# Optimization experiments

Hardware: AMD Instinct MI355X
Metric: run time of the kernel (lower is better)

Reference implementation:

```python
import jax, jax.numpy as jnp
import numpy as np

WS = (5, 5, 5, 5)  # 4D window

def _rel_index(ws):
    # faithful port of WindowAttention.relative_bias_4d
    coords = np.stack(np.meshgrid(*[np.arange(w) for w in ws], indexing='ij'))  # (4, H,W,Hs,Ws)
    flat = coords.reshape(len(ws), -1)                       # (4, N)
    rel = (flat[:, :, None] - flat[:, None, :]).transpose(1, 2, 0).astype(np.int64)  # (N, N, 4)
    rel = rel + np.array([ws[0] - 1, ws[1] - 1, ws[2] - 1, ws[3] - 1])
    rel[..., 0] *= (2 * ws[0] - 1) ** 3
    rel[..., 1] *= (2 * ws[1] - 1) ** 2
    rel[..., 2] *= (2 * ws[2] - 1)
    return rel.sum(-1)  # (N, N), values in [0, (2w-1)^4)


def setup_inputs() -> dict:
    key = jax.random.key(0)
    ks = jax.random.split(key, 7)
    dim, heads = 128, 4
    B_, nW = 64, 32
    N = 5 ** 4  # 625
    tbl = (2 * 5 - 1) ** 4  # 6561
    inp = {
        'x': jax.random.normal(ks[0], (B_, N, dim), jnp.float32),
        'mask': jax.random.normal(ks[1], (nW, N, N), jnp.float32),
        'qkv_w': jax.random.normal(ks[2], (3 * dim, dim), jnp.float32) * 0.02,
        'qkv_b': jax.random.normal(ks[3], (3 * dim,), jnp.float32) * 0.02,
        'proj_w': jax.random.normal(ks[4], (dim, dim), jnp.float32) * 0.02,
        'proj_b': jax.random.normal(ks[5], (dim,), jnp.float32) * 0.02,
        'bias_table': jax.random.normal(ks[6], (tbl, heads), jnp.float32) * 0.02,
        'rel_index': jnp.asarray(_rel_index(WS), jnp.int32),
    }
    return inp


def reference(x, mask, qkv_w, qkv_b, proj_w, proj_b, bias_table, rel_index):
    B_, N, C = x.shape
    H = bias_table.shape[-1]
    D = C // H
    scale = D ** -0.5
    # qkv projection -> (3, B_, H, N, D)
    qkv = (x @ qkv_w.T + qkv_b).reshape(B_, N, 3, H, D).transpose(2, 0, 3, 1, 4)
    q, k, v = qkv[0], qkv[1], qkv[2]
    attn = jnp.einsum('bhnd,bhmd->bhnm', q * scale, k)       # (B_, H, N, N)
    bias = bias_table[rel_index].transpose(2, 0, 1)          # (H, N, N)
    attn = attn + bias[None]
    nW = mask.shape[0]
    attn = attn.reshape(B_ // nW, nW, H, N, N) + mask[None, :, None]
    attn = jax.nn.softmax(attn.reshape(B_, H, N, N), axis=-1)
    out = jnp.einsum('bhnm,bhmd->bhnd', attn, v)             # (B_, H, N, D)
    out = out.transpose(0, 2, 1, 3).reshape(B_, N, C)
    return out @ proj_w.T + proj_b
```

## Files before the change

### kernel.cpp

```cpp
#include <hip/hip_runtime.h>
#include <stdint.h>

typedef __attribute__((ext_vector_type(8))) __bf16 bf16x8;
typedef __attribute__((ext_vector_type(4))) __bf16 bf16x4;
typedef __attribute__((ext_vector_type(4))) float f32x4;

#define DEV __device__ __forceinline__
#define LOG2E 1.4426950408889634f
#define SCALE 0.17677669529663687f

static constexpr size_t OFF_Q     = 0;
static constexpr size_t OFF_K     = 10485760;
static constexpr size_t OFF_VT    = 20971520;
static constexpr size_t OFF_O     = 31457280;
static constexpr size_t OFF_BIASP = 41697280;
static constexpr size_t OFF_WBF   = 44974080;

DEV bf16x8 cvt8(const float* p) {
  f32x4 a = *(const f32x4*)p;
  f32x4 b = *(const f32x4*)(p + 4);
  bf16x8 r;
  r[0]=(__bf16)a[0]; r[1]=(__bf16)a[1]; r[2]=(__bf16)a[2]; r[3]=(__bf16)a[3];
  r[4]=(__bf16)b[0]; r[5]=(__bf16)b[1]; r[6]=(__bf16)b[2]; r[7]=(__bf16)b[3];
  return r;
}

DEV f32x4 mfma16(bf16x8 a, bf16x8 b, f32x4 c) {
  return __builtin_amdgcn_mfma_f32_16x16x32_bf16(a, b, c, 0, 0, 0);
}

DEV void gload16(const float* g, float* l) {
  typedef const __attribute__((address_space(1))) uint32_t* gp_t;
  typedef __attribute__((address_space(3))) uint32_t* lp_t;
  __builtin_amdgcn_global_load_lds((gp_t)g, (lp_t)l, 16, 0, 0);
}

__global__ __launch_bounds__(256) void k_prep(const float* __restrict__ table,
                                              const int* __restrict__ rel,
                                              __bf16* __restrict__ bp,
                                              __bf16* __restrict__ qp,
                                              __bf16* __restrict__ kp,
                                              __bf16* __restrict__ vp,
                                              const float* __restrict__ wq,
                                              const float* __restrict__ wp,
                                              __bf16* __restrict__ wbf) {
  int blk = blockIdx.x;
  if (blk < 1600) {
    int t = blk * 256 + threadIdx.x;
    int h = t / 102400, rem = t % 102400;
    int i = rem / 160, j4 = (rem % 160) * 4;
    bf16x4 v;
    if (i < 625) {
      #pragma unroll
      for (int r = 0; r < 4; ++r) {
        int j = j4 + r;
        v[r] = (j < 625) ? (__bf16)(table[(size_t)rel[(size_t)i * 625 + j] * 4 + h] * LOG2E)
                         : (__bf16)0.f;
      }
    } else {
      v[0] = v[1] = v[2] = v[3] = (__bf16)0.f;
    }
    *(bf16x4*)(bp + ((size_t)h * 640 + i) * 640 + j4) = v;
  } else if (blk < 2560) {
    int t = (blk - 1600) * 256 + threadIdx.x;
    const int PAD1 = 256 * 15 * 32;
    if (t < PAD1) {
      int bh = t / 480, rem = t % 480;
      int row = 625 + rem / 32, d = rem & 31;
      size_t idx = ((size_t)bh * 640 + row) * 32 + d;
      qp[idx] = (__bf16)0.f;
      kp[idx] = (__bf16)0.f;
    } else {
      t -= PAD1;
      if (t < PAD1) {
        int bh = t / 480, rem = t % 480;
        int d = rem / 15, col = 625 + rem % 15;
        vp[((size_t)bh * 32 + d) * 640 + col] = (__bf16)0.f;
      }
    }
  } else {
    int t = (blk - 2560) * 256 + threadIdx.x;
    if (t < 49152) wbf[t] = (__bf16)wq[t];
    else           wbf[t] = (__bf16)wp[t - 49152];
  }
}

__global__ __launch_bounds__(256) void k_qkv(const float* __restrict__ x,
                                             const __bf16* __restrict__ wbf,
                                             const float* __restrict__ bias,
                                             __bf16* __restrict__ qp,
                                             __bf16* __restrict__ kp,
                                             __bf16* __restrict__ vp) {
  int lane = threadIdx.x & 63, wv = threadIdx.x >> 6;
  int g = lane >> 4, l15 = lane & 15;
  int row0 = (blockIdx.x * 4 + wv) * 16;

  bf16x8 a[4];
  #pragma unroll
  for (int ks = 0; ks < 4; ++ks)
    a[ks] = cvt8(x + (size_t)(row0 + l15) * 128 + ks * 32 + g * 8);

  #pragma unroll 1
  for (int nf = 0; nf < 24; ++nf) {
    f32x4 acc = {0.f, 0.f, 0.f, 0.f};
    int col = nf * 16 + l15;
    #pragma unroll
    for (int ks = 0; ks < 4; ++ks) {
      bf16x8 bfr = *(const bf16x8*)(wbf + (size_t)col * 128 + ks * 32 + g * 8);
      acc = mfma16(a[ks], bfr, acc);
    }
    float bv = bias[col];
    int which = nf >> 3;
    int h = (col >> 5) & 3, d = col & 31;
    #pragma unroll
    for (int r = 0; r < 4; ++r) {
      int row = row0 + 4 * g + r;
      int b_ = row / 625;
      int n = row - b_ * 625;
      float v = acc[r] + bv;
      size_t bh = (size_t)b_ * 4 + h;
      if (which == 0)       qp[(bh * 640 + n) * 32 + d] = (__bf16)(v * (SCALE * LOG2E));
      else if (which == 1)  kp[(bh * 640 + n) * 32 + d] = (__bf16)v;
      else                  vp[(bh * 32 + d) * 640 + n] = (__bf16)v;
    }
  }
}

__global__ __launch_bounds__(256, 4) void k_attn6(const __bf16* __restrict__ qball,
                                                  const __bf16* __restrict__ kball,
                                                  const __bf16* __restrict__ vball,
                                                  __bf16* __restrict__ oball,
                                                  const __bf16* __restrict__ biasp,
                                                  const float* __restrict__ maskraw) {
  __shared__ __align__(16) float Mbuf[2][32 * 32];
  __shared__ __align__(16) unsigned short Pl[4][32 * 56];

  const int tid = threadIdx.x;
  const int lane = tid & 63, wv = tid >> 6;
  const int g = lane >> 4, l15 = lane & 15;

  const int bid = blockIdx.x;
  const int xcd = bid & 7, s = bid >> 3;
  const int w = xcd + 8 * (s & 3);
  const int r_ = s >> 2;
  const int o = r_ & 1, chunk = r_ >> 1;
  const int b = o * 32 + w;
  const int h = wv;
  const size_t bh = (size_t)b * 4 + h;
  const int i0 = chunk * 32;

  const __bf16* qp = qball + bh * (640 * 32);
  const __bf16* kp = kball + bh * (640 * 32);
  const __bf16* vp = vball + bh * (32 * 640);
  const float* maskw = maskraw + (size_t)w * 390625;

  const __bf16* kbase  = kp + (size_t)l15 * 32 + g * 8;
  const __bf16* vbase0 = vp + (size_t)l15 * 640 + 8 * g;
  const __bf16* vbase1 = vp + (size_t)(16 + l15) * 640 + 8 * g;
  const __bf16* brow0  = biasp + (size_t)h * 409600 + (size_t)(i0 + l15) * 640 + 4 * g;
  const __bf16* brow1  = brow0 + 16 * 640;

  const int il_s = wv * 8 + (lane >> 3);
  const int gr_s = (lane & 7) ^ (il_s & 7);
  int row_s = i0 + il_s; row_s = row_s < 625 ? row_s : 624;
  const float* msrc = maskw + (size_t)row_s * 625 + gr_s * 4;
  float* mdst0 = &Mbuf[0][wv * 256];
  float* mdst1 = &Mbuf[1][wv * 256];

  bf16x8 aq0 = *(const bf16x8*)(qp + (size_t)(i0 + l15) * 32 + g * 8);
  bf16x8 aq1 = *(const bf16x8*)(qp + (size_t)(i0 + 16 + l15) * 32 + g * 8);

  unsigned short* Prow0 = &Pl[wv][l15 * 56];
  unsigned short* Prow1 = &Pl[wv][(16 + l15) * 56];

  f32x4 O00 = {0,0,0,0}, O01 = {0,0,0,0}, O10 = {0,0,0,0}, O11 = {0,0,0,0};
  float L0 = 0.f, L1 = 0.f;

  bf16x8 K0, K1;
  bf16x4 B00, B01, B10, B11;

  gload16(msrc, mdst0);
  K0  = *(const bf16x8*)(kbase);
  K1  = *(const bf16x8*)(kbase + 512);
  B00 = *(const bf16x4*)(brow0);
  B01 = *(const bf16x4*)(brow0 + 16);
  B10 = *(const bf16x4*)(brow1);
  B11 = *(const bf16x4*)(brow1 + 16);
  __syncthreads();

#define CORE(BUF, T)                                                           \
  {                                                                            \
                                       \
    bf16x8 v0 = *(const bf16x8*)(vbase0 + (T) * 32);                           \
    bf16x8 v1 = *(const bf16x8*)(vbase1 + (T) * 32);                           \
    const int swz = (l15 & 7) << 2;                                            \
    f32x4 c00 = *(const f32x4*)&Mbuf[BUF][l15 * 32 + ((4 * g) ^ swz)];         \
    f32x4 c01 = *(const f32x4*)&Mbuf[BUF][l15 * 32 + ((16 + 4 * g) ^ swz)];    \
    f32x4 c10 = *(const f32x4*)&Mbuf[BUF][(16 + l15) * 32 + ((4 * g) ^ swz)];  \
    f32x4 c11 = *(const f32x4*)&Mbuf[BUF][(16 + l15) * 32 + ((16 + 4 * g) ^ swz)]; \
    _Pragma("unroll")                                                          \
    for (int r = 0; r < 4; ++r) {                                              \
      c00[r] = fmaf(c00[r], LOG2E, (float)B00[r]);                             \
      c01[r] = fmaf(c01[r], LOG2E, (float)B01[r]);                             \
      c10[r] = fmaf(c10[r], LOG2E, (float)B10[r]);                             \
      c11[r] = fmaf(c11[r], LOG2E, (float)B11[r]);                             \
    }                                                                          \
    f32x4 S00 = mfma16(K0, aq0, c00);                                          \
    f32x4 S01 = mfma16(K1, aq0, c01);                                          \
    f32x4 S10 = mfma16(K0, aq1, c10);                                          \
    f32x4 S11 = mfma16(K1, aq1, c11);                                          \
    if ((T) < 19) {   \
      K0  = *(const bf16x8*)(kbase + (size_t)((T) + 1) * 1024);                \
      K1  = *(const bf16x8*)(kbase + (size_t)((T) + 1) * 1024 + 512);          \
      B00 = *(const bf16x4*)(brow0 + ((T) + 1) * 32);                          \
      B01 = *(const bf16x4*)(brow0 + ((T) + 1) * 32 + 16);                     \
      B10 = *(const bf16x4*)(brow1 + ((T) + 1) * 32);                          \
      B11 = *(const bf16x4*)(brow1 + ((T) + 1) * 32 + 16);                     \
    }                                                                          \
    float ps0 = 0.f, ps1 = 0.f;                                                \
    bf16x4 pk00, pk01, pk10, pk11;                                             \
    _Pragma("unroll")                                                          \
    for (int r = 0; r < 4; ++r) {                                              \
      float p00 = exp2f(S00[r]);                                               \
      float p01 = exp2f(S01[r]);                                               \
      float p10 = exp2f(S10[r]);                                               \
      float p11 = exp2f(S11[r]);                                               \
      ps0 += p00 + p01;                                                        \
      ps1 += p10 + p11;                                                        \
      pk00[r] = (__bf16)p00;                                                   \
      pk01[r] = (__bf16)p01;                                                   \
      pk10[r] = (__bf16)p10;                                                   \
      pk11[r] = (__bf16)p11;                                                   \
    }                                                                          \
    L0 += ps0; L1 += ps1;                                                      \
    *(bf16x4*)(Prow0 + 4 * g) = pk00;                                          \
    *(bf16x4*)(Prow0 + 16 + 4 * g) = pk01;                                     \
    *(bf16x4*)(Prow1 + 4 * g) = pk10;                                          \
    *(bf16x4*)(Prow1 + 16 + 4 * g) = pk11;                                     \
    bf16x8 pa0 = *(const bf16x8*)(Prow0 + 8 * g);                              \
    bf16x8 pa1 = *(const bf16x8*)(Prow1 + 8 * g);                              \
    O00 = mfma16(pa0, v0, O00);                                                \
    O01 = mfma16(pa0, v1, O01);                                                \
    O10 = mfma16(pa1, v0, O10);                                                \
    O11 = mfma16(pa1, v1, O11);                                                \
  }

  #pragma unroll 1
  for (int t = 0; t < 18; ++t) {
    gload16(msrc + (size_t)(t + 1) * 32, (t & 1) ? mdst0 : mdst1);
    CORE(t & 1, t)
    __syncthreads();
  }
  CORE(0, 18)

  {
    bf16x8 v0 = *(const bf16x8*)(vbase0 + 19 * 32);
    bf16x8 v1 = *(const bf16x8*)(vbase1 + 19 * 32);
    int i_a = i0 + l15;       int ir0 = i_a < 625 ? i_a : 624;
    int i_b = i0 + 16 + l15;  int ir1 = i_b < 625 ? i_b : 624;
    const float* mr0 = maskw + (size_t)ir0 * 625;
    const float* mr1 = maskw + (size_t)ir1 * 625;
    f32x4 c, S00, S01, S10, S11;
    #pragma unroll
    for (int r = 0; r < 4; ++r)
      c[r] = fmaf(mr0[608 + 4 * g + r], LOG2E, (float)B00[r]);
    S00 = mfma16(K0, aq0, c);
    #pragma unroll
    for (int r = 0; r < 4; ++r) {
      int j = 624 + 4 * g + r;
      c[r] = (j < 625) ? fmaf(mr0[j], LOG2E, (float)B01[r]) : -1.0e30f;
    }
    S01 = mfma16(K1, aq0, c);
    #pragma unroll
    for (int r = 0; r < 4; ++r)
      c[r] = fmaf(mr1[608 + 4 * g + r], LOG2E, (float)B10[r]);
    S10 = mfma16(K0, aq1, c);
    #pragma unroll
    for (int r = 0; r < 4; ++r) {
      int j = 624 + 4 * g + r;
      c[r] = (j < 625) ? fmaf(mr1[j], LOG2E, (float)B11[r]) : -1.0e30f;
    }
    S11 = mfma16(K1, aq1, c);

    float ps0 = 0.f, ps1 = 0.f;
    bf16x4 pk00, pk01, pk10, pk11;
    #pragma unroll
    for (int r = 0; r < 4; ++r) {
      float p00 = exp2f(S00[r]);
      float p01 = exp2f(S01[r]);
      float p10 = exp2f(S10[r]);
      float p11 = exp2f(S11[r]);
      ps0 += p00 + p01;
      ps1 += p10 + p11;
      pk00[r] = (__bf16)p00;
      pk01[r] = (__bf16)p01;
      pk10[r] = (__bf16)p10;
      pk11[r] = (__bf16)p11;
    }
    L0 += ps0; L1 += ps1;
    *(bf16x4*)(Prow0 + 4 * g) = pk00;
    *(bf16x4*)(Prow0 + 16 + 4 * g) = pk01;
    *(bf16x4*)(Prow1 + 4 * g) = pk10;
    *(bf16x4*)(Prow1 + 16 + 4 * g) = pk11;
    bf16x8 pa0 = *(const bf16x8*)(Prow0 + 8 * g);
    bf16x8 pa1 = *(const bf16x8*)(Prow1 + 8 * g);
    O00 = mfma16(pa0, v0, O00);
    O01 = mfma16(pa0, v1, O01);
    O10 = mfma16(pa1, v0, O10);
    O11 = mfma16(pa1, v1, O11);
  }
#undef CORE

  L0 += __shfl_xor(L0, 16); L0 += __shfl_xor(L0, 32);
  L1 += __shfl_xor(L1, 16); L1 += __shfl_xor(L1, 32);
  float inv0 = 1.0f / L0, inv1 = 1.0f / L1;
  f32x4 iv0, iv1;
  #pragma unroll
  for (int r = 0; r < 4; ++r) {
    iv0[r] = __shfl(inv0, 4 * g + r);
    iv1[r] = __shfl(inv1, 4 * g + r);
  }
  #pragma unroll
  for (int r = 0; r < 4; ++r) {
    int ia = i0 + 4 * g + r;
    if (ia < 625) {
      size_t base = ((size_t)b * 625 + ia) * 128 + h * 32;
      oball[base + l15]      = (__bf16)(O00[r] * iv0[r]);
      oball[base + 16 + l15] = (__bf16)(O01[r] * iv0[r]);
    }
    int ib = i0 + 16 + 4 * g + r;
    if (ib < 625) {
      size_t base = ((size_t)b * 625 + ib) * 128 + h * 32;
      oball[base + l15]      = (__bf16)(O10[r] * iv1[r]);
      oball[base + 16 + l15] = (__bf16)(O11[r] * iv1[r]);
    }
  }
}

__global__ __launch_bounds__(256) void k_proj(const __bf16* __restrict__ obf,
                                              const __bf16* __restrict__ wbf,
                                              const float* __restrict__ bias,
                                              float* __restrict__ out) {
  int lane = threadIdx.x & 63, wv = threadIdx.x >> 6;
  int g = lane >> 4, l15 = lane & 15;
  int row0 = (blockIdx.x * 4 + wv) * 16;

  bf16x8 a[4];
  #pragma unroll
  for (int ks = 0; ks < 4; ++ks)
    a[ks] = *(const bf16x8*)(obf + (size_t)(row0 + l15) * 128 + ks * 32 + g * 8);

  #pragma unroll 1
  for (int nf = 0; nf < 8; ++nf) {
    f32x4 acc = {0.f, 0.f, 0.f, 0.f};
    int col = nf * 16 + l15;
    #pragma unroll
    for (int ks = 0; ks < 4; ++ks) {
      bf16x8 bfr = *(const bf16x8*)(wbf + (size_t)col * 128 + ks * 32 + g * 8);
      acc = mfma16(a[ks], bfr, acc);
    }
    float bv = bias[col];
    #pragma unroll
    for (int r = 0; r < 4; ++r)
      out[(size_t)(row0 + 4 * g + r) * 128 + col] = acc[r] + bv;
  }
}

extern "C" void kernel_launch(void* const* d_in, const int* in_sizes, int n_in,
                              void* d_out, int out_size, void* d_ws, size_t ws_size,
                              hipStream_t stream) {
  (void)in_sizes; (void)n_in; (void)out_size; (void)ws_size;
  const float* x      = (const float*)d_in[0];
  const float* mask   = (const float*)d_in[1];
  const float* qkv_w  = (const float*)d_in[2];
  const float* qkv_b  = (const float*)d_in[3];
  const float* proj_w = (const float*)d_in[4];
  const float* proj_b = (const float*)d_in[5];
  const float* table  = (const float*)d_in[6];
  const int*   rel    = (const int*)d_in[7];
  char* ws = (char*)d_ws;
  float* out = (float*)d_out;

  __bf16* qp    = (__bf16*)(ws + OFF_Q);
  __bf16* kp    = (__bf16*)(ws + OFF_K);
  __bf16* vp    = (__bf16*)(ws + OFF_VT);
  __bf16* obf   = (__bf16*)(ws + OFF_O);
  __bf16* biasp = (__bf16*)(ws + OFF_BIASP);
  __bf16* wbf   = (__bf16*)(ws + OFF_WBF);

  k_prep<<<2816, 256, 0, stream>>>(table, rel, biasp, qp, kp, vp, qkv_w, proj_w, wbf);
  k_qkv<<<625, 256, 0, stream>>>(x, wbf, qkv_b, qp, kp, vp);
  k_attn6<<<1280, 256, 0, stream>>>(qp, kp, vp, obf, biasp, mask);
  k_proj<<<625, 256, 0, stream>>>(obf, wbf + 49152, proj_b, out);
}
```

Baseline: 162.1 us.

## Load mask directly into registers and permute bias layout for 8-wide loads

The attention kernel stops staging the mask tile through double-buffered LDS with async global-to-LDS loads and per-tile block barriers. Each lane now reads its mask values straight from global memory into registers, prefetching one tile ahead. The precomputed bias array is reordered so each lane fetches a single 8-element bf16 vector per row instead of two 4-element loads. This removes the block-wide synchronisation and LDS traffic, at the cost of more register pressure and less coalesced mask reads.

New measurement: 157.2 us. -3.1%, faster.

```diff
diff --git a/kernel.cpp b/kernel.cpp
--- a/kernel.cpp
+++ b/kernel.cpp
@@ -27,12 +27,6 @@
 
 DEV f32x4 mfma16(bf16x8 a, bf16x8 b, f32x4 c) {
   return __builtin_amdgcn_mfma_f32_16x16x32_bf16(a, b, c, 0, 0, 0);
-}
-
-DEV void gload16(const float* g, float* l) {
-  typedef const __attribute__((address_space(1))) uint32_t* gp_t;
-  typedef __attribute__((address_space(3))) uint32_t* lp_t;
-  __builtin_amdgcn_global_load_lds((gp_t)g, (lp_t)l, 16, 0, 0);
 }
 
 __global__ __launch_bounds__(256) void k_prep(const float* __restrict__ table,
@@ -48,19 +42,22 @@
   if (blk < 1600) {
     int t = blk * 256 + threadIdx.x;
     int h = t / 102400, rem = t % 102400;
-    int i = rem / 160, j4 = (rem % 160) * 4;
+    int i = rem / 160, q = rem % 160;
+    int e0 = q * 4;
+    int tile = e0 >> 5;
+    int ein = e0 & 31;
+    int g = ein >> 3, s0 = ein & 7;
     bf16x4 v;
-    if (i < 625) {
-      #pragma unroll
-      for (int r = 0; r < 4; ++r) {
-        int j = j4 + r;
-        v[r] = (j < 625) ? (__bf16)(table[(size_t)rel[(size_t)i * 625 + j] * 4 + h] * LOG2E)
-                         : (__bf16)0.f;
-      }
-    } else {
-      v[0] = v[1] = v[2] = v[3] = (__bf16)0.f;
-    }
-    *(bf16x4*)(bp + ((size_t)h * 640 + i) * 640 + j4) = v;
+    #pragma unroll
+    for (int s2 = 0; s2 < 4; ++s2) {
+      int s = s0 + s2;
+      int col = 4 * g + (s < 4 ? s : s + 12);
+      int j = tile * 32 + col;
+      v[s2] = (i < 625 && j < 625)
+                ? (__bf16)(table[(size_t)rel[(size_t)i * 625 + j] * 4 + h] * LOG2E)
+                : (__bf16)0.f;
+    }
+    *(bf16x4*)(bp + ((size_t)h * 640 + i) * 640 + e0) = v;
   } else if (blk < 2560) {
     int t = (blk - 1600) * 256 + threadIdx.x;
     const int PAD1 = 256 * 15 * 32;
@@ -126,13 +123,12 @@
   }
 }
 
-__global__ __launch_bounds__(256, 4) void k_attn6(const __bf16* __restrict__ qball,
+__global__ __launch_bounds__(256, 4) void k_attn8(const __bf16* __restrict__ qball,
                                                   const __bf16* __restrict__ kball,
                                                   const __bf16* __restrict__ vball,
                                                   __bf16* __restrict__ oball,
                                                   const __bf16* __restrict__ biasp,
                                                   const float* __restrict__ maskraw) {
-  __shared__ __align__(16) float Mbuf[2][32 * 32];
   __shared__ __align__(16) unsigned short Pl[4][32 * 56];
 
   const int tid = threadIdx.x;
@@ -157,15 +153,13 @@
   const __bf16* kbase  = kp + (size_t)l15 * 32 + g * 8;
   const __bf16* vbase0 = vp + (size_t)l15 * 640 + 8 * g;
   const __bf16* vbase1 = vp + (size_t)(16 + l15) * 640 + 8 * g;
-  const __bf16* brow0  = biasp + (size_t)h * 409600 + (size_t)(i0 + l15) * 640 + 4 * g;
+  const __bf16* brow0  = biasp + (size_t)h * 409600 + (size_t)(i0 + l15) * 640 + g * 8;
   const __bf16* brow1  = brow0 + 16 * 640;
 
-  const int il_s = wv * 8 + (lane >> 3);
-  const int gr_s = (lane & 7) ^ (il_s & 7);
-  int row_s = i0 + il_s; row_s = row_s < 625 ? row_s : 624;
-  const float* msrc = maskw + (size_t)row_s * 625 + gr_s * 4;
-  float* mdst0 = &Mbuf[0][wv * 256];
-  float* mdst1 = &Mbuf[1][wv * 256];
+  int ia = i0 + l15;       const int ir0 = ia < 625 ? ia : 624;
+  int ib_ = i0 + 16 + l15; const int ir1 = ib_ < 625 ? ib_ : 624;
+  const float* mrow0 = maskw + (size_t)ir0 * 625 + 4 * g;
+  const float* mrow1 = maskw + (size_t)ir1 * 625 + 4 * g;
 
   bf16x8 aq0 = *(const bf16x8*)(qp + (size_t)(i0 + l15) * 32 + g * 8);
   bf16x8 aq1 = *(const bf16x8*)(qp + (size_t)(i0 + 16 + l15) * 32 + g * 8);
@@ -177,110 +171,44 @@
   float L0 = 0.f, L1 = 0.f;
 
   bf16x8 K0, K1;
-  bf16x4 B00, B01, B10, B11;
-
-  gload16(msrc, mdst0);
+  bf16x8 B0, B1;
+  f32x4 C00, C01, C10, C11;
+
+  C00 = *(const f32x4*)(mrow0);
+  C01 = *(const f32x4*)(mrow0 + 16);
+  C10 = *(const f32x4*)(mrow1);
+  C11 = *(const f32x4*)(mrow1 + 16);
   K0  = *(const bf16x8*)(kbase);
   K1  = *(const bf16x8*)(kbase + 512);
-  B00 = *(const bf16x4*)(brow0);
-  B01 = *(const bf16x4*)(brow0 + 16);
-  B10 = *(const bf16x4*)(brow1);
-  B11 = *(const bf16x4*)(brow1 + 16);
-  __syncthreads();
-
-#define CORE(BUF, T)                                                           \
-  {                                                                            \
-                                       \
-    bf16x8 v0 = *(const bf16x8*)(vbase0 + (T) * 32);                           \
-    bf16x8 v1 = *(const bf16x8*)(vbase1 + (T) * 32);                           \
-    const int swz = (l15 & 7) << 2;                                            \
-    f32x4 c00 = *(const f32x4*)&Mbuf[BUF][l15 * 32 + ((4 * g) ^ swz)];         \
-    f32x4 c01 = *(const f32x4*)&Mbuf[BUF][l15 * 32 + ((16 + 4 * g) ^ swz)];    \
-    f32x4 c10 = *(const f32x4*)&Mbuf[BUF][(16 + l15) * 32 + ((4 * g) ^ swz)];  \
-    f32x4 c11 = *(const f32x4*)&Mbuf[BUF][(16 + l15) * 32 + ((16 + 4 * g) ^ swz)]; \
-    _Pragma("unroll")                                                          \
-    for (int r = 0; r < 4; ++r) {                                              \
-      c00[r] = fmaf(c00[r], LOG2E, (float)B00[r]);                             \
-      c01[r] = fmaf(c01[r], LOG2E, (float)B01[r]);                             \
-      c10[r] = fmaf(c10[r], LOG2E, (float)B10[r]);                             \
-      c11[r] = fmaf(c11[r], LOG2E, (float)B11[r]);                             \
-    }                                                                          \
-    f32x4 S00 = mfma16(K0, aq0, c00);                                          \
-    f32x4 S01 = mfma16(K1, aq0, c01);                                          \
-    f32x4 S10 = mfma16(K0, aq1, c10);                                          \
-    f32x4 S11 = mfma16(K1, aq1, c11);                                          \
-    if ((T) < 19) {   \
-      K0  = *(const bf16x8*)(kbase + (size_t)((T) + 1) * 1024);                \
-      K1  = *(const bf16x8*)(kbase + (size_t)((T) + 1) * 1024 + 512);          \
-      B00 = *(const bf16x4*)(brow0 + ((T) + 1) * 32);                          \
-      B01 = *(const bf16x4*)(brow0 + ((T) + 1) * 32 + 16);                     \
-      B10 = *(const bf16x4*)(brow1 + ((T) + 1) * 32);                          \
-      B11 = *(const bf16x4*)(brow1 + ((T) + 1) * 32 + 16);                     \
-    }                                                                          \
-    float ps0 = 0.f, ps1 = 0.f;                                                \
-    bf16x4 pk00, pk01, pk10, pk11;                                             \
-    _Pragma("unroll")                                                          \
-    for (int r = 0; r < 4; ++r) {                                              \
-      float p00 = exp2f(S00[r]);                                               \
-      float p01 = exp2f(S01[r]);                                               \
-      float p10 = exp2f(S10[r]);                                               \
-      float p11 = exp2f(S11[r]);                                               \
-      ps0 += p00 + p01;                                                        \
-      ps1 += p10 + p11;                                                        \
-      pk00[r] = (__bf16)p00;                                                   \
-      pk01[r] = (__bf16)p01;                                                   \
-      pk10[r] = (__bf16)p10;                                                   \
-      pk11[r] = (__bf16)p11;                                                   \
-    }                                                                          \
-    L0 += ps0; L1 += ps1;                                                      \
-    *(bf16x4*)(Prow0 + 4 * g) = pk00;                                          \
-    *(bf16x4*)(Prow0 + 16 + 4 * g) = pk01;                                     \
-    *(bf16x4*)(Prow1 + 4 * g) = pk10;                                          \
-    *(bf16x4*)(Prow1 + 16 + 4 * g) = pk11;                                     \
-    bf16x8 pa0 = *(const bf16x8*)(Prow0 + 8 * g);                              \
-    bf16x8 pa1 = *(const bf16x8*)(Prow1 + 8 * g);                              \
-    O00 = mfma16(pa0, v0, O00);                                                \
-    O01 = mfma16(pa0, v1, O01);                                                \
-    O10 = mfma16(pa1, v0, O10);                                                \
-    O11 = mfma16(pa1, v1, O11);                                                \
-  }
+  B0  = *(const bf16x8*)(brow0);
+  B1  = *(const bf16x8*)(brow1);
 
   #pragma unroll 1
-  for (int t = 0; t < 18; ++t) {
-    gload16(msrc + (size_t)(t + 1) * 32, (t & 1) ? mdst0 : mdst1);
-    CORE(t & 1, t)
-    __syncthreads();
-  }
-  CORE(0, 18)
-
-  {
-    bf16x8 v0 = *(const bf16x8*)(vbase0 + 19 * 32);
-    bf16x8 v1 = *(const bf16x8*)(vbase1 + 19 * 32);
-    int i_a = i0 + l15;       int ir0 = i_a < 625 ? i_a : 624;
-    int i_b = i0 + 16 + l15;  int ir1 = i_b < 625 ? i_b : 624;
-    const float* mr0 = maskw + (size_t)ir0 * 625;
-    const float* mr1 = maskw + (size_t)ir1 * 625;
-    f32x4 c, S00, S01, S10, S11;
-    #pragma unroll
-    for (int r = 0; r < 4; ++r)
-      c[r] = fmaf(mr0[608 + 4 * g + r], LOG2E, (float)B00[r]);
-    S00 = mfma16(K0, aq0, c);
-    #pragma unroll
-    for (int r = 0; r < 4; ++r) {
-      int j = 624 + 4 * g + r;
-      c[r] = (j < 625) ? fmaf(mr0[j], LOG2E, (float)B01[r]) : -1.0e30f;
-    }
-    S01 = mfma16(K1, aq0, c);
-    #pragma unroll
-    for (int r = 0; r < 4; ++r)
-      c[r] = fmaf(mr1[608 + 4 * g + r], LOG2E, (float)B10[r]);
-    S10 = mfma16(K0, aq1, c);
-    #pragma unroll
-    for (int r = 0; r < 4; ++r) {
-      int j = 624 + 4 * g + r;
-      c[r] = (j < 625) ? fmaf(mr1[j], LOG2E, (float)B11[r]) : -1.0e30f;
-    }
-    S11 = mfma16(K1, aq1, c);
+  for (int t = 0; t < 19; ++t) {
+    bf16x8 v0 = *(const bf16x8*)(vbase0 + t * 32);
+    bf16x8 v1 = *(const bf16x8*)(vbase1 + t * 32);
+    f32x4 c00, c01, c10, c11;
+    #pragma unroll
+    for (int r = 0; r < 4; ++r) {
+      c00[r] = fmaf(C00[r], LOG2E, (float)B0[r]);
+      c01[r] = fmaf(C01[r], LOG2E, (float)B0[4 + r]);
+      c10[r] = fmaf(C10[r], LOG2E, (float)B1[r]);
+      c11[r] = fmaf(C11[r], LOG2E, (float)B1[4 + r]);
+    }
+    f32x4 S00 = mfma16(K0, aq0, c00);
+    f32x4 S01 = mfma16(K1, aq0, c01);
+    f32x4 S10 = mfma16(K0, aq1, c10);
+    f32x4 S11 = mfma16(K1, aq1, c11);
+    if (t < 18) {
+      C00 = *(const f32x4*)(mrow0 + (t + 1) * 32);
+      C01 = *(const f32x4*)(mrow0 + (t + 1) * 32 + 16);
+      C10 = *(const f32x4*)(mrow1 + (t + 1) * 32);
+      C11 = *(const f32x4*)(mrow1 + (t + 1) * 32 + 16);
+    }
+    K0 = *(const bf16x8*)(kbase + (size_t)(t + 1) * 1024);
+    K1 = *(const bf16x8*)(kbase + (size_t)(t + 1) * 1024 + 512);
+    B0 = *(const bf16x8*)(brow0 + (t + 1) * 32);
+    B1 = *(const bf16x8*)(brow1 + (t + 1) * 32);
 
     float ps0 = 0.f, ps1 = 0.f;
     bf16x4 pk00, pk01, pk10, pk11;
@@ -309,7 +237,61 @@
     O10 = mfma16(pa1, v0, O10);
     O11 = mfma16(pa1, v1, O11);
   }
-#undef CORE
+
+  {
+    bf16x8 v0 = *(const bf16x8*)(vbase0 + 19 * 32);
+    bf16x8 v1 = *(const bf16x8*)(vbase1 + 19 * 32);
+    const float* mr0 = maskw + (size_t)ir0 * 625;
+    const float* mr1 = maskw + (size_t)ir1 * 625;
+    f32x4 c, S00, S01, S10, S11;
+    #pragma unroll
+    for (int r = 0; r < 4; ++r)
+      c[r] = fmaf(mr0[608 + 4 * g + r], LOG2E, (float)B0[r]);
+    S00 = mfma16(K0, aq0, c);
+    #pragma unroll
+    for (int r = 0; r < 4; ++r) {
+      int j = 624 + 4 * g + r;
+      c[r] = (j < 625) ? fmaf(mr0[j], LOG2E, (float)B0[4 + r]) : -1.0e30f;
+    }
+    S01 = mfma16(K1, aq0, c);
+    #pragma unroll
+    for (int r = 0; r < 4; ++r)
+      c[r] = fmaf(mr1[608 + 4 * g + r], LOG2E, (float)B1[r]);
+    S10 = mfma16(K0, aq1, c);
+    #pragma unroll
+    for (int r = 0; r < 4; ++r) {
+      int j = 624 + 4 * g + r;
+      c[r] = (j < 625) ? fmaf(mr1[j], LOG2E, (float)B1[4 + r]) : -1.0e30f;
+    }
+    S11 = mfma16(K1, aq1, c);
+
+    float ps0 = 0.f, ps1 = 0.f;
+    bf16x4 pk00, pk01, pk10, pk11;
+    #pragma unroll
+    for (int r = 0; r < 4; ++r) {
+      float p00 = exp2f(S00[r]);
+      float p01 = exp2f(S01[r]);
+      float p10 = exp2f(S10[r]);
+      float p11 = exp2f(S11[r]);
+      ps0 += p00 + p01;
+      ps1 += p10 + p11;
+      pk00[r] = (__bf16)p00;
+      pk01[r] = (__bf16)p01;
+      pk10[r] = (__bf16)p10;
+      pk11[r] = (__bf16)p11;
+    }
+    L0 += ps0; L1 += ps1;
+    *(bf16x4*)(Prow0 + 4 * g) = pk00;
+    *(bf16x4*)(Prow0 + 16 + 4 * g) = pk01;
+    *(bf16x4*)(Prow1 + 4 * g) = pk10;
+    *(bf16x4*)(Prow1 + 16 + 4 * g) = pk11;
+    bf16x8 pa0 = *(const bf16x8*)(Prow0 + 8 * g);
+    bf16x8 pa1 = *(const bf16x8*)(Prow1 + 8 * g);
+    O00 = mfma16(pa0, v0, O00);
+    O01 = mfma16(pa0, v1, O01);
+    O10 = mfma16(pa1, v0, O10);
+    O11 = mfma16(pa1, v1, O11);
+  }
 
   L0 += __shfl_xor(L0, 16); L0 += __shfl_xor(L0, 32);
   L1 += __shfl_xor(L1, 16); L1 += __shfl_xor(L1, 32);
@@ -322,15 +304,15 @@
   }
   #pragma unroll
   for (int r = 0; r < 4; ++r) {
-    int ia = i0 + 4 * g + r;
-    if (ia < 625) {
-      size_t base = ((size_t)b * 625 + ia) * 128 + h * 32;
+    int ia2 = i0 + 4 * g + r;
+    if (ia2 < 625) {
+      size_t base = ((size_t)b * 625 + ia2) * 128 + h * 32;
       oball[base + l15]      = (__bf16)(O00[r] * iv0[r]);
       oball[base + 16 + l15] = (__bf16)(O01[r] * iv0[r]);
     }
-    int ib = i0 + 16 + 4 * g + r;
-    if (ib < 625) {
-      size_t base = ((size_t)b * 625 + ib) * 128 + h * 32;
+    int ib2 = i0 + 16 + 4 * g + r;
+    if (ib2 < 625) {
+      size_t base = ((size_t)b * 625 + ib2) * 128 + h * 32;
       oball[base + l15]      = (__bf16)(O10[r] * iv1[r]);
       oball[base + 16 + l15] = (__bf16)(O11[r] * iv1[r]);
     }
@@ -390,6 +372,6 @@
 
   k_prep<<<2816, 256, 0, stream>>>(table, rel, biasp, qp, kp, vp, qkv_w, proj_w, wbf);
   k_qkv<<<625, 256, 0, stream>>>(x, wbf, qkv_b, qp, kp, vp);
-  k_attn6<<<1280, 256, 0, stream>>>(qp, kp, vp, obf, biasp, mask);
+  k_attn8<<<1280, 256, 0, stream>>>(qp, kp, vp, obf, biasp, mask);
   k_proj<<<625, 256, 0, stream>>>(obf, wbf + 49152, proj_b, out);
 }
```
